# Kernel tuning notes

Hardware: AMD Instinct MI355X
Metric: run time of the kernel (lower is better)

Reference implementation:

```python
import jax, jax.numpy as jnp
import numpy as np

N_TOKEN = 256
C_PAIR = 128
C = 32
N_HEADS = 4
LN_EPS = 1e-5


def setup_inputs() -> dict:
    key = jax.random.key(0)
    ks = jax.random.split(key, 8)
    w = lambda k, shape: jax.random.normal(k, shape, dtype=jnp.float32) * 0.02
    return {
        "pair": jax.random.normal(ks[0], (N_TOKEN, N_TOKEN, C_PAIR), dtype=jnp.float32),
        "gamma": jnp.ones((C_PAIR,), dtype=jnp.float32),
        "beta": jnp.zeros((C_PAIR,), dtype=jnp.float32),
        "Wq": w(ks[1], (C_PAIR, C * N_HEADS)),
        "Wk": w(ks[2], (C_PAIR, C * N_HEADS)),
        "Wv": w(ks[3], (C_PAIR, C * N_HEADS)),
        "Wb": w(ks[4], (C_PAIR, N_HEADS)),
        "Wg": w(ks[5], (C_PAIR, C * N_HEADS)),
        "Wout": w(ks[6], (C * N_HEADS, C_PAIR)),
    }


def _layernorm(x, gamma, beta):
    mu = jnp.mean(x, axis=-1, keepdims=True)
    var = jnp.mean(jnp.square(x - mu), axis=-1, keepdims=True)
    return (x - mu) * jax.lax.rsqrt(var + LN_EPS) * gamma + beta


def reference(pair, gamma, beta, Wq, Wk, Wv, Wb, Wg, Wout):
    n = pair.shape[0]
    pn = _layernorm(pair, gamma, beta)  # [N, N, c_pair]
    q = (pn @ Wq).reshape(n, n, N_HEADS, C)  # [i, j, h, c]
    k = (pn @ Wk).reshape(n, n, N_HEADS, C)  # [i, k, h, c]
    v = (pn @ Wv).reshape(n, n, N_HEADS, C)
    b = pn @ Wb                               # [j, k, h] pairwise bias
    g = jax.nn.sigmoid(pn @ Wg).reshape(n, n, N_HEADS, C)
    # a^h_ijk = softmax_k( q_ij . k_ik / sqrt(c) + b_jk )
    logits = jnp.einsum("ijhc,ikhc->ijkh", q, k) / np.float32(np.sqrt(C))
    logits = logits + b[None, :, :, :]        # broadcast over i: bias indexed by (j, k)
    attn = jax.nn.softmax(logits, axis=2)     # softmax over k axis
    o = jnp.einsum("ijkh,ikhc->ijhc", attn, v) * g
    return o.reshape(n, n, N_HEADS * C) @ Wout  # [N, N, c_pair]
```

## Files before the change

### kernel.cpp

```cpp
#include <hip/hip_runtime.h>

#define N_TOK 256
#define CP    128
#define CHD   32
#define NH    4
#define NT    65536
#define NCOL  528

typedef short short8 __attribute__((ext_vector_type(8)));
typedef float f32x4  __attribute__((ext_vector_type(4)));

__device__ __forceinline__ short f2bf(float f) {
    unsigned u = __builtin_bit_cast(unsigned, f);
    u += 0x7fffu + ((u >> 16) & 1u);
    return (short)(u >> 16);
}
__device__ __forceinline__ float bf2f(short s) {
    unsigned u = ((unsigned)(unsigned short)s) << 16;
    return __builtin_bit_cast(float, u);
}

__global__ void pack_weights(const float* __restrict__ Wq, const float* __restrict__ Wk,
                             const float* __restrict__ Wv, const float* __restrict__ Wb,
                             const float* __restrict__ Wg, const float* __restrict__ Wout,
                             short* __restrict__ wcat, short* __restrict__ woutT) {
    int idx = blockIdx.x * 256 + threadIdx.x;
    if (idx < NCOL * CP) {
        int n = idx >> 7, k = idx & 127;
        float v = 0.f;
        if (n < 512) {
            const float* W = (n < 128) ? Wq : (n < 256) ? Wk : (n < 384) ? Wv : Wg;
            int col = (n & 96) + 2 * (n & 15) + ((n >> 4) & 1);
            v = W[k * 128 + col];
        } else if (n < 516) {
            v = Wb[k * 4 + (n - 512)];
        }
        wcat[n * CP + k] = f2bf(v);
    } else {
        int j = idx - NCOL * CP;
        if (j < 128 * 128) {
            int n = j >> 7, k = j & 127;
            woutT[n * 128 + k] = f2bf(Wout[k * 128 + n]);
        }
    }
}

__global__ __launch_bounds__(256, 4)
void ln_proj(const float* __restrict__ pair, const float* __restrict__ gamma,
             const float* __restrict__ beta, const short* __restrict__ wcat,
             short* __restrict__ qt, short* __restrict__ kt,
             short* __restrict__ vt, short* __restrict__ gt,
             float* __restrict__ bt) {
    __shared__ short pn[64 * 136];
    const int tid = threadIdx.x;
    const int wv = tid >> 6, lane = tid & 63;
    const int quad = lane >> 4, l15 = lane & 15;
    const int r0 = blockIdx.x * 64;

    float ga0 = gamma[2 * lane], ga1 = gamma[2 * lane + 1];
    float be0 = beta[2 * lane],  be1 = beta[2 * lane + 1];

    #pragma unroll 4
    for (int rr = 0; rr < 16; ++rr) {
        int row = wv * 16 + rr;
        const float* src = pair + (size_t)(r0 + row) * CP + 2 * lane;
        float x0 = src[0], x1 = src[1];
        float s = x0 + x1;
        #pragma unroll
        for (int m = 32; m; m >>= 1) s += __shfl_xor(s, m);
        float mu = s * (1.f / 128.f);
        float d0 = x0 - mu, d1 = x1 - mu;
        float vs = d0 * d0 + d1 * d1;
        #pragma unroll
        for (int m = 32; m; m >>= 1) vs += __shfl_xor(vs, m);
        float rs = rsqrtf(vs * (1.f / 128.f) + 1e-5f);
        short y0 = f2bf(d0 * rs * ga0 + be0);
        short y1 = f2bf(d1 * rs * ga1 + be1);
        unsigned pk = ((unsigned)(unsigned short)y0) | (((unsigned)(unsigned short)y1) << 16);
        *(unsigned*)&pn[row * 136 + 2 * lane] = pk;
    }
    __syncthreads();

    short8 af[4][4];
    #pragma unroll
    for (int rt = 0; rt < 4; ++rt)
        #pragma unroll
        for (int s = 0; s < 4; ++s)
            af[rt][s] = *(const short8*)&pn[(rt * 16 + l15) * 136 + s * 32 + quad * 8];

    short* const dst = (wv == 0) ? qt : (wv == 1) ? kt : (wv == 2) ? vt : gt;

#define LOADB(BUF, CHN) {                                                          \
        int n_ = (CHN) * 16 + l15;                                                 \
        _Pragma("unroll")                                                          \
        for (int s = 0; s < 4; ++s)                                                \
            BUF[s] = *(const short8*)&wcat[(size_t)n_ * CP + s * 32 + quad * 8];   \
    }

#define EVEN(BUF) {                                                                \
        _Pragma("unroll")                                                          \
        for (int rt = 0; rt < 4; ++rt) {                                           \
            f32x4 a = {0.f, 0.f, 0.f, 0.f};                                        \
            _Pragma("unroll")                                                      \
            for (int s = 0; s < 4; ++s)                                            \
                a = __builtin_amdgcn_mfma_f32_16x16x32_bf16(af[rt][s], BUF[s], a, 0, 0, 0); \
            accE[rt] = a;                                                          \
        }                                                                          \
    }

#define ODD(CC, BUF) {                                                             \
        const int chn = wv * 8 + (CC);                                             \
        const int h_ = (chn >> 1) & 3;                                             \
        const size_t hb = (size_t)h_ * NT * CHD + 2 * l15;                         \
        _Pragma("unroll")                                                          \
        for (int rt = 0; rt < 4; ++rt) {                                           \
            f32x4 a = {0.f, 0.f, 0.f, 0.f};                                        \
            _Pragma("unroll")                                                      \
            for (int s = 0; s < 4; ++s)                                            \
                a = __builtin_amdgcn_mfma_f32_16x16x32_bf16(af[rt][s], BUF[s], a, 0, 0, 0); \
            _Pragma("unroll")                                                      \
            for (int r = 0; r < 4; ++r) {                                          \
                int gr = r0 + rt * 16 + quad * 4 + r;                              \
                float ve = accE[rt][r], vo = a[r];                                 \
                if (wv == 3) {                                                     \
                    ve = 1.f / (1.f + __expf(-ve));                                \
                    vo = 1.f / (1.f + __expf(-vo));                                \
                }                                                                  \
                unsigned pk = ((unsigned)(unsigned short)f2bf(ve))                 \
                            | (((unsigned)(unsigned short)f2bf(vo)) << 16);        \
                *(unsigned*)&dst[hb + (size_t)gr * CHD] = pk;                      \
            }                                                                      \
        }                                                                          \
    }

    short8 bA[4], bB[4];
    f32x4 accE[4];
    LOADB(bA, wv * 8 + 0)
    LOADB(bB, wv * 8 + 1)
    EVEN(bA) LOADB(bA, wv * 8 + 2)
    ODD(1, bB) LOADB(bB, wv * 8 + 3)
    EVEN(bA) LOADB(bA, wv * 8 + 4)
    ODD(3, bB) LOADB(bB, wv * 8 + 5)
    EVEN(bA) LOADB(bA, wv * 8 + 6)
    ODD(5, bB) LOADB(bB, wv * 8 + 7)
    EVEN(bA) LOADB(bA, wv * 8 + 8)
    ODD(7, bB)

    if (wv == 3) {
        #pragma unroll
        for (int rt = 0; rt < 4; ++rt) {
            f32x4 acc = {0.f, 0.f, 0.f, 0.f};
            #pragma unroll
            for (int s = 0; s < 4; ++s)
                acc = __builtin_amdgcn_mfma_f32_16x16x32_bf16(af[rt][s], bA[s], acc, 0, 0, 0);
            if (l15 < 4) {
                #pragma unroll
                for (int r = 0; r < 4; ++r) {
                    int gr = r0 + rt * 16 + quad * 4 + r;
                    bt[l15 * NT + gr] = acc[r];
                }
            }
        }
    }
#undef LOADB
#undef EVEN
#undef ODD
}

__global__ __launch_bounds__(256)
void attn(const short* __restrict__ qt, const short* __restrict__ kt,
          const short* __restrict__ vt, const short* __restrict__ gt,
          const float* __restrict__ bt, short* __restrict__ og) {
    __shared__ short vT[32 * 264];
    __shared__ short pl[64 * 264];
    const int tid = threadIdx.x;
    const int h = blockIdx.x >> 8, i = blockIdx.x & 255;
    const int wv = tid >> 6, lane = tid & 63;
    const int quad = lane >> 4, l15 = lane & 15;

    const short* kbase = kt + ((size_t)h * NT + (size_t)i * 256) * CHD;
    const short* vbase = vt + ((size_t)h * NT + (size_t)i * 256) * CHD;
    const short* qbase = qt + ((size_t)h * NT + (size_t)i * 256) * CHD;
    const short* gbase = gt + ((size_t)h * NT + (size_t)i * 256) * CHD;
    const float* bbase = bt + (size_t)h * NT;

    for (int g = tid; g < 1024; g += 256) {
        int key = g >> 2, p = g & 3;
        short8 s = *(const short8*)(vbase + key * CHD + p * 8);
        #pragma unroll
        for (int cc = 0; cc < 8; ++cc)
            vT[(p * 8 + cc) * 264 + key] = s[cc];
    }
    __syncthreads();

    const float scale = 0.17677669529663687f;

    for (int jt = 0; jt < 4; ++jt) {
        int jbase = jt * 64 + wv * 16;
        short8 aq = *(const short8*)(qbase + (jbase + l15) * CHD + quad * 8);

        f32x4 sacc[16];
        #pragma unroll
        for (int t = 0; t < 16; ++t) {
            short8 bk = *(const short8*)(kbase + (t * 16 + l15) * CHD + quad * 8);
            f32x4 z = {0.f, 0.f, 0.f, 0.f};
            sacc[t] = __builtin_amdgcn_mfma_f32_16x16x32_bf16(aq, bk, z, 0, 0, 0);
        }
        #pragma unroll
        for (int t = 0; t < 16; ++t)
            #pragma unroll
            for (int r = 0; r < 4; ++r) {
                int j = jbase + quad * 4 + r;
                sacc[t][r] = sacc[t][r] * scale + bbase[(size_t)j * 256 + t * 16 + l15];
            }
        float mx[4] = {-1e30f, -1e30f, -1e30f, -1e30f}, sm[4] = {0.f, 0.f, 0.f, 0.f};
        #pragma unroll
        for (int t = 0; t < 16; ++t)
            #pragma unroll
            for (int r = 0; r < 4; ++r) mx[r] = fmaxf(mx[r], sacc[t][r]);
        #pragma unroll
        for (int m = 1; m < 16; m <<= 1)
            #pragma unroll
            for (int r = 0; r < 4; ++r) mx[r] = fmaxf(mx[r], __shfl_xor(mx[r], m, 16));
        #pragma unroll
        for (int t = 0; t < 16; ++t)
            #pragma unroll
            for (int r = 0; r < 4; ++r) {
                float e = __expf(sacc[t][r] - mx[r]);
                sacc[t][r] = e;
                sm[r] += e;
            }
        #pragma unroll
        for (int m = 1; m < 16; m <<= 1)
            #pragma unroll
            for (int r = 0; r < 4; ++r) sm[r] += __shfl_xor(sm[r], m, 16);
        float inv[4];
        #pragma unroll
        for (int r = 0; r < 4; ++r) inv[r] = 1.f / sm[r];
        #pragma unroll
        for (int t = 0; t < 16; ++t)
            #pragma unroll
            for (int r = 0; r < 4; ++r)
                pl[(wv * 16 + quad * 4 + r) * 264 + t * 16 + l15] = f2bf(sacc[t][r] * inv[r]);
        __syncthreads();
        f32x4 oacc[2];
        oacc[0] = f32x4{0.f, 0.f, 0.f, 0.f};
        oacc[1] = f32x4{0.f, 0.f, 0.f, 0.f};
        #pragma unroll
        for (int ks = 0; ks < 8; ++ks) {
            short8 ap = *(const short8*)&pl[(wv * 16 + l15) * 264 + ks * 32 + quad * 8];
            #pragma unroll
            for (int nt = 0; nt < 2; ++nt) {
                short8 bv = *(const short8*)&vT[(nt * 16 + l15) * 264 + ks * 32 + quad * 8];
                oacc[nt] = __builtin_amdgcn_mfma_f32_16x16x32_bf16(ap, bv, oacc[nt], 0, 0, 0);
            }
        }
        #pragma unroll
        for (int nt = 0; nt < 2; ++nt) {
            int c = nt * 16 + l15;
            #pragma unroll
            for (int r = 0; r < 4; ++r) {
                int j = jbase + quad * 4 + r;
                float gv = bf2f(gbase[(size_t)j * CHD + c]);
                float o = oacc[nt][r] * gv;
                og[((size_t)i * 256 + j) * CP + h * CHD + c] = f2bf(o);
            }
        }
        __syncthreads();
    }
}

__global__ __launch_bounds__(256)
void out_gemm(const short* __restrict__ og, const short* __restrict__ woutT,
              float* __restrict__ out) {
    __shared__ short al[64 * 136];
    const int tid = threadIdx.x;
    const int wv = tid >> 6, lane = tid & 63;
    const int quad = lane >> 4, l15 = lane & 15;
    const int r0 = blockIdx.x * 64;

    for (int g = tid; g < 1024; g += 256) {
        int row = g >> 4, p = g & 15;
        *(short8*)&al[row * 136 + p * 8] = *(const short8*)(og + (size_t)(r0 + row) * CP + p * 8);
    }
    __syncthreads();

    short8 af[4];
    #pragma unroll
    for (int s = 0; s < 4; ++s)
        af[s] = *(const short8*)&al[(wv * 16 + l15) * 136 + s * 32 + quad * 8];

    #pragma unroll
    for (int ch = 0; ch < 8; ++ch) {
        int n = ch * 16 + l15;
        f32x4 acc = {0.f, 0.f, 0.f, 0.f};
        #pragma unroll
        for (int s = 0; s < 4; ++s) {
            short8 bfrag = *(const short8*)&woutT[(size_t)n * 128 + s * 32 + quad * 8];
            acc = __builtin_amdgcn_mfma_f32_16x16x32_bf16(af[s], bfrag, acc, 0, 0, 0);
        }
        #pragma unroll
        for (int r = 0; r < 4; ++r)
            out[(size_t)(r0 + wv * 16 + quad * 4 + r) * CP + n] = acc[r];
    }
}

extern "C" void kernel_launch(void* const* d_in, const int* in_sizes, int n_in,
                              void* d_out, int out_size, void* d_ws, size_t ws_size,
                              hipStream_t stream) {
    (void)in_sizes; (void)n_in; (void)out_size; (void)ws_size;
    const float* pair  = (const float*)d_in[0];
    const float* gamma = (const float*)d_in[1];
    const float* beta  = (const float*)d_in[2];
    const float* Wq    = (const float*)d_in[3];
    const float* Wk    = (const float*)d_in[4];
    const float* Wv    = (const float*)d_in[5];
    const float* Wb    = (const float*)d_in[6];
    const float* Wg    = (const float*)d_in[7];
    const float* Wout  = (const float*)d_in[8];
    float* out = (float*)d_out;

    char* ws = (char*)d_ws;
    const size_t SZ_QKVG = (size_t)NH * NT * CHD * 2;
    short* wcat  = (short*)(ws);
    short* woutT = (short*)(ws + 135168);
    short* qt    = (short*)(ws + 167936);
    short* kt    = (short*)(ws + 167936 + SZ_QKVG);
    short* vt    = (short*)(ws + 167936 + 2 * SZ_QKVG);
    short* gt    = (short*)(ws + 167936 + 3 * SZ_QKVG);
    float* bt    = (float*)(ws + 167936 + 4 * SZ_QKVG);
    short* og    = (short*)(ws + 167936 + 4 * SZ_QKVG + (size_t)NH * NT * 4);

    hipLaunchKernelGGL(pack_weights, dim3(328), dim3(256), 0, stream,
                       Wq, Wk, Wv, Wb, Wg, Wout, wcat, woutT);
    hipLaunchKernelGGL(ln_proj, dim3(1024), dim3(256), 0, stream,
                       pair, gamma, beta, wcat, qt, kt, vt, gt, bt);
    hipLaunchKernelGGL(attn, dim3(1024), dim3(256), 0, stream,
                       qt, kt, vt, gt, bt, og);
    hipLaunchKernelGGL(out_gemm, dim3(1024), dim3(256), 0, stream,
                       og, woutT, out);
}
```

Baseline: 210.7 us.

## Fold scale into Wq, bias into MFMA accumulator, drop syncs, pack gated stores

Folds the 1/sqrt(c) softmax scale into the packed Wq weights and feeds the pairwise bias as the MFMA accumulator input, so the separate scale-and-add pass disappears. It permutes the V transpose rows so each lane's two output columns are adjacent, which lets the gate load and the bf16 output store become packed 32-bit accesses. Both __syncthreads in the j-tile loop are removed because each wave only touches its own P rows and vT is read-only after setup. s_setprio hints are added around the MFMA sections. Dropping the barriers relies on per-wave data ownership, and the bf16 rounding of Q now happens after scaling.

```diff
diff --git a/kernel.cpp b/kernel.cpp
--- a/kernel.cpp
+++ b/kernel.cpp
@@ -32,6 +32,7 @@
             const float* W = (n < 128) ? Wq : (n < 256) ? Wk : (n < 384) ? Wv : Wg;
             int col = (n & 96) + 2 * (n & 15) + ((n >> 4) & 1);
             v = W[k * 128 + col];
+            if (n < 128) v *= 0.17677669529663687f;
         } else if (n < 516) {
             v = Wb[k * 4 + (n - 512)];
         }
@@ -188,31 +189,30 @@
         int key = g >> 2, p = g & 3;
         short8 s = *(const short8*)(vbase + key * CHD + p * 8);
         #pragma unroll
-        for (int cc = 0; cc < 8; ++cc)
-            vT[(p * 8 + cc) * 264 + key] = s[cc];
+        for (int cc = 0; cc < 8; ++cc) {
+            int c = p * 8 + cc;
+            int row = (c & 1) ? 16 + (c >> 1) : (c >> 1);
+            vT[row * 264 + key] = s[cc];
+        }
     }
     __syncthreads();
-
-    const float scale = 0.17677669529663687f;
 
     for (int jt = 0; jt < 4; ++jt) {
         int jbase = jt * 64 + wv * 16;
         short8 aq = *(const short8*)(qbase + (jbase + l15) * CHD + quad * 8);
 
         f32x4 sacc[16];
+        __builtin_amdgcn_s_setprio(1);
         #pragma unroll
         for (int t = 0; t < 16; ++t) {
+            f32x4 c;
+            #pragma unroll
+            for (int r = 0; r < 4; ++r)
+                c[r] = bbase[(size_t)(jbase + quad * 4 + r) * 256 + t * 16 + l15];
             short8 bk = *(const short8*)(kbase + (t * 16 + l15) * CHD + quad * 8);
-            f32x4 z = {0.f, 0.f, 0.f, 0.f};
-            sacc[t] = __builtin_amdgcn_mfma_f32_16x16x32_bf16(aq, bk, z, 0, 0, 0);
-        }
-        #pragma unroll
-        for (int t = 0; t < 16; ++t)
-            #pragma unroll
-            for (int r = 0; r < 4; ++r) {
-                int j = jbase + quad * 4 + r;
-                sacc[t][r] = sacc[t][r] * scale + bbase[(size_t)j * 256 + t * 16 + l15];
-            }
+            sacc[t] = __builtin_amdgcn_mfma_f32_16x16x32_bf16(aq, bk, c, 0, 0, 0);
+        }
+        __builtin_amdgcn_s_setprio(0);
         float mx[4] = {-1e30f, -1e30f, -1e30f, -1e30f}, sm[4] = {0.f, 0.f, 0.f, 0.f};
         #pragma unroll
         for (int t = 0; t < 16; ++t)
@@ -242,10 +242,10 @@
             #pragma unroll
             for (int r = 0; r < 4; ++r)
                 pl[(wv * 16 + quad * 4 + r) * 264 + t * 16 + l15] = f2bf(sacc[t][r] * inv[r]);
-        __syncthreads();
         f32x4 oacc[2];
         oacc[0] = f32x4{0.f, 0.f, 0.f, 0.f};
         oacc[1] = f32x4{0.f, 0.f, 0.f, 0.f};
+        __builtin_amdgcn_s_setprio(1);
         #pragma unroll
         for (int ks = 0; ks < 8; ++ks) {
             short8 ap = *(const short8*)&pl[(wv * 16 + l15) * 264 + ks * 32 + quad * 8];
@@ -255,18 +255,17 @@
                 oacc[nt] = __builtin_amdgcn_mfma_f32_16x16x32_bf16(ap, bv, oacc[nt], 0, 0, 0);
             }
         }
-        #pragma unroll
-        for (int nt = 0; nt < 2; ++nt) {
-            int c = nt * 16 + l15;
-            #pragma unroll
-            for (int r = 0; r < 4; ++r) {
-                int j = jbase + quad * 4 + r;
-                float gv = bf2f(gbase[(size_t)j * CHD + c]);
-                float o = oacc[nt][r] * gv;
-                og[((size_t)i * 256 + j) * CP + h * CHD + c] = f2bf(o);
-            }
-        }
-        __syncthreads();
+        __builtin_amdgcn_s_setprio(0);
+        #pragma unroll
+        for (int r = 0; r < 4; ++r) {
+            int j = jbase + quad * 4 + r;
+            unsigned gw = *(const unsigned*)(gbase + (size_t)j * CHD + 2 * l15);
+            float g0 = bf2f((short)(gw & 0xffff));
+            float g1 = bf2f((short)(gw >> 16));
+            unsigned pk = ((unsigned)(unsigned short)f2bf(oacc[0][r] * g0))
+                        | (((unsigned)(unsigned short)f2bf(oacc[1][r] * g1)) << 16);
+            *(unsigned*)&og[((size_t)i * 256 + j) * CP + h * CHD + 2 * l15] = pk;
+        }
     }
 }
 
```

Result: faster. 206.2 us (-2.1%).
